# Kernel optimization log

Measured on AMD Instinct MI355X. Metric: run time of the kernel, lower is better.

Reference implementation:

```python
import jax, jax.numpy as jnp
import numpy as np

NUM_EXPERTS = 8
TOP_K = 2

def setup_inputs() -> dict:
    key = jax.random.key(0)
    ks = jax.random.split(key, 5)
    B, S, D, F, E = 4, 2048, 1024, 4096, NUM_EXPERTS
    x = jax.random.normal(ks[0], (B, S, D), dtype=jnp.float32)
    router_w = jax.random.normal(ks[1], (D, E), dtype=jnp.float32) * 0.02
    router_b = jnp.zeros((E,), dtype=jnp.float32)
    w1 = jax.random.normal(ks[2], (E, D, F), dtype=jnp.float32) * 0.02
    b1 = jnp.zeros((E, F), dtype=jnp.float32)
    w2 = jax.random.normal(ks[3], (E, F, D), dtype=jnp.float32) * 0.02
    b2 = jnp.zeros((E, D), dtype=jnp.float32)
    return {"x": x, "router_w": router_w, "router_b": router_b,
            "w1": w1, "b1": b1, "w2": w2, "b2": b2}

def reference(x, router_w, router_b, w1, b1, w2, b2):
    B, S, D = x.shape
    E = router_w.shape[1]
    x_flat = x.reshape(-1, D)                                  # [N, D]
    router_probs = jax.nn.softmax(x_flat @ router_w + router_b, axis=-1)  # [N, E]
    topk_probs, topk_idx = jax.lax.top_k(router_probs, TOP_K)  # [N, K]
    topk_probs = topk_probs / jnp.sum(topk_probs, axis=-1, keepdims=True)
    # combine weight per (token, expert): sum over top-k slots assigned to that expert
    cw = jnp.sum(topk_probs[..., None] * jax.nn.one_hot(topk_idx, E, dtype=x.dtype), axis=1)  # [N, E]
    out = jnp.zeros_like(x_flat)
    for e in range(E):  # small fixed expert count; each iter is a dense GEMM pair
        h = jax.nn.gelu(x_flat @ w1[e] + b1[e], approximate=False)  # [N, F]
        out = out + cw[:, e:e + 1] * (h @ w2[e] + b2[e])            # [N, D]
    return out.reshape(B, S, D)
```

## Files before the change

kernel.cpp:

```cpp
#include <hip/hip_runtime.h>
#include <hip/hip_bf16.h>

typedef __attribute__((ext_vector_type(8))) __bf16 bf16x8;
typedef __attribute__((ext_vector_type(4))) float f32x4;

#define NTOK 8192
#define D_DIM 1024
#define F_DIM 4096
#define NEXP 8
#define SLOT_TOT 16384
#define SLOT_CAP 16640
#define TILE_MAX 136
#define TILE_MAX2 72

__device__ __forceinline__ unsigned short f2b(float f) {
  __hip_bfloat16 b = __float2bfloat16(f);
  return reinterpret_cast<unsigned short&>(b);
}

__device__ __forceinline__ float gelu_f(float v) {
  const float y2 = v * (1.5957691216f + 0.0713548162f * v * v);
  return v * __builtin_amdgcn_rcpf(1.f + __expf(-y2));
}

__device__ __forceinline__ void gload_lds16(const void* g, void* l) {
  __builtin_amdgcn_global_load_lds(
      (__attribute__((address_space(1))) void*)g,
      (__attribute__((address_space(3))) void*)l, 16, 0, 0);
}


__global__ void init_counts_kernel(int* counts) {
  if (threadIdx.x < NEXP) counts[threadIdx.x] = 0;
}

__global__ void zero_out_kernel(float* out) {
  const int i = blockIdx.x * 256 + threadIdx.x;
  reinterpret_cast<float4*>(out)[i] = make_float4(0.f, 0.f, 0.f, 0.f);
}

__global__ void scatter_gather_kernel(const float* __restrict__ x,
                                      const int* __restrict__ topk_idx,
                                      int* __restrict__ cursors,
                                      int* __restrict__ slot_pos,
                                      __hip_bfloat16* __restrict__ xg) {
  __shared__ int ps[2];
  const int tok = blockIdx.x;
  const int tid = threadIdx.x;
  if (tid < 2) {
    const int e = topk_idx[tok * 2 + tid];
    const int p = atomicAdd(&cursors[e], 1);
    slot_pos[tok * 2 + tid] = p;
    ps[tid] = p;
  }
  __syncthreads();
  const int d = tid * 4;
  const float4 v = *reinterpret_cast<const float4*>(x + (size_t)tok * D_DIM + d);
  union { unsigned short u[4]; uint2 q; } o;
  o.u[0] = f2b(v.x); o.u[1] = f2b(v.y); o.u[2] = f2b(v.z); o.u[3] = f2b(v.w);
  *reinterpret_cast<uint2*>(xg + (size_t)ps[0] * D_DIM + d) = o.q;
  *reinterpret_cast<uint2*>(xg + (size_t)ps[1] * D_DIM + d) = o.q;
}

__global__ void combine_kernel(const __hip_bfloat16* __restrict__ ys,
                               const int* __restrict__ slot_pos,
                               const float* __restrict__ topk_w,
                               float* __restrict__ out) {
  const int tok = blockIdx.x;
  const int d = threadIdx.x * 4;
  const int s0 = slot_pos[tok * 2], s1 = slot_pos[tok * 2 + 1];
  const float w0 = topk_w[tok * 2], w1 = topk_w[tok * 2 + 1];
  union { unsigned short u[4]; uint2 q; } a, b;
  a.q = *reinterpret_cast<const uint2*>(ys + (size_t)s0 * D_DIM + d);
  b.q = *reinterpret_cast<const uint2*>(ys + (size_t)s1 * D_DIM + d);
  float4 rr;
  float va[4];
  #pragma unroll
  for (int i = 0; i < 4; ++i) {
    unsigned int ua = (unsigned int)a.u[i] << 16;
    unsigned int ub = (unsigned int)b.u[i] << 16;
    va[i] = w0 * reinterpret_cast<float&>(ua) + w1 * reinterpret_cast<float&>(ub);
  }
  rr.x = va[0]; rr.y = va[1]; rr.z = va[2]; rr.w = va[3];
  *reinterpret_cast<float4*>(out + (size_t)tok * D_DIM + d) = rr;
}

__global__ void transpose_conv_kernel(const float* __restrict__ src,
                                      __hip_bfloat16* __restrict__ dst,
                                      int R, int C) {
  __shared__ float tile[64][65];
  const int e = blockIdx.z;
  src += (size_t)e * R * C;
  dst += (size_t)e * R * C;
  const int c0 = blockIdx.x * 64, r0 = blockIdx.y * 64;
  const int tid = threadIdx.x;
  const int lr = tid >> 4, lc4 = (tid & 15) * 4;
  #pragma unroll
  for (int pass = 0; pass < 4; ++pass) {
    const int rr = pass * 16 + lr;
    const float4 v = *reinterpret_cast<const float4*>(
        &src[(size_t)(r0 + rr) * C + c0 + lc4]);
    tile[rr][lc4 + 0] = v.x; tile[rr][lc4 + 1] = v.y;
    tile[rr][lc4 + 2] = v.z; tile[rr][lc4 + 3] = v.w;
  }
  __syncthreads();
  const int sc = tid >> 3, sr8 = (tid & 7) * 8;
  #pragma unroll
  for (int pass = 0; pass < 2; ++pass) {
    const int c = pass * 32 + sc;
    union { unsigned short u[8]; uint4 q; } o;
    #pragma unroll
    for (int i = 0; i < 8; ++i) o.u[i] = f2b(tile[sr8 + i][c]);
    *reinterpret_cast<uint4*>(&dst[(size_t)(c0 + c) * R + r0 + sr8]) = o.q;
  }
}

__global__ void router_kernel(const float* __restrict__ x,
                              const float* __restrict__ rw,
                              const float* __restrict__ rb,
                              int* __restrict__ topk_idx,
                              float* __restrict__ topk_w,
                              int* __restrict__ counts) {
  __shared__ float rwT[NEXP * D_DIM];
  const int tid = threadIdx.x;
  for (int i = tid; i < NEXP * D_DIM; i += 256) {
    const int d = i >> 3, e = i & 7;
    rwT[e * D_DIM + d] = rw[i];
  }
  __syncthreads();

  const int wave = tid >> 6, lane = tid & 63;
  const int tok = blockIdx.x * 4 + wave;
  const float* xr = x + (size_t)tok * D_DIM;

  float acc[NEXP];
  #pragma unroll
  for (int e = 0; e < NEXP; ++e) acc[e] = 0.f;

  for (int i = 0; i < D_DIM / 64; ++i) {
    const int d = i * 64 + lane;
    const float xv = xr[d];
    #pragma unroll
    for (int e = 0; e < NEXP; ++e) acc[e] += xv * rwT[e * D_DIM + d];
  }
  #pragma unroll
  for (int off = 32; off > 0; off >>= 1) {
    #pragma unroll
    for (int e = 0; e < NEXP; ++e) acc[e] += __shfl_xor(acc[e], off);
  }

  if (lane == 0) {
    float l[NEXP];
    #pragma unroll
    for (int e = 0; e < NEXP; ++e) l[e] = acc[e] + rb[e];
    int i1 = 0;
    #pragma unroll
    for (int e = 1; e < NEXP; ++e) if (l[e] > l[i1]) i1 = e;
    int i2 = (i1 == 0) ? 1 : 0;
    #pragma unroll
    for (int e = 0; e < NEXP; ++e) if (e != i1 && e != i2 && l[e] > l[i2]) i2 = e;
    const float w1 = 1.f / (1.f + __expf(l[i2] - l[i1]));
    topk_idx[tok * 2 + 0] = i1;
    topk_idx[tok * 2 + 1] = i2;
    topk_w[tok * 2 + 0] = w1;
    topk_w[tok * 2 + 1] = 1.f - w1;
    atomicAdd(&counts[i1], 1);
    atomicAdd(&counts[i2], 1);
  }
}

__global__ void offsets_kernel(const int* __restrict__ counts,
                               int* __restrict__ offsets,
                               int* __restrict__ cursors,
                               int* __restrict__ tile_meta,
                               int* __restrict__ tile_meta2) {
  if (threadIdx.x == 0) {
    int s = 0;
    for (int e = 0; e < NEXP; ++e) { offsets[e] = s; cursors[e] = s; s += counts[e]; }
    offsets[NEXP] = s;
    int n = 0;
    for (int e = 0; e < NEXP; ++e) {
      const int nt = (counts[e] + 127) >> 7;
      for (int m = 0; m < nt && n < TILE_MAX; ++m) tile_meta[n++] = e | (m << 8);
    }
    for (; n < TILE_MAX; ++n) tile_meta[n] = 0 | (1 << 22);
    n = 0;
    for (int e = 0; e < NEXP; ++e) {
      const int nt = (counts[e] + 255) >> 8;
      for (int m = 0; m < nt && n < TILE_MAX2; ++m) tile_meta2[n++] = e | (m << 8);
    }
    for (; n < TILE_MAX2; ++n) tile_meta2[n] = 0 | (1 << 22);
  }
}

__global__ __launch_bounds__(512, 2) void moe_gemm1(
    const __hip_bfloat16* __restrict__ A,
    const __hip_bfloat16* __restrict__ B,
    const float* __restrict__ bias,
    const int* __restrict__ counts,
    const int* __restrict__ offsets,
    const int* __restrict__ tile_meta2,
    __hip_bfloat16* __restrict__ Hout) {
  constexpr int K = D_DIM, NCOL = F_DIM;
  constexpr int KT = K / 64;

  const int bid = blockIdx.x;
  const int j = bid >> 4, nt = bid & 15;
  const int meta = tile_meta2[j];
  const int e = meta & 255, mt = meta >> 8;
  const int cnt = counts[e];
  if (mt * 256 >= cnt) return;
  const int base = offsets[e];

  __shared__ unsigned short lds[2][32768];

  const int tid = threadIdx.x;
  const int w = tid >> 6, lane = tid & 63;
  const int r = lane & 15, kg = lane >> 4;
  const int wm = w >> 2, wn = w & 3;

  const __hip_bfloat16* gA0 = A + (size_t)(base + mt * 256 + w * 16 + r) * K + kg * 8;
  const __hip_bfloat16* gA1 = gA0 + (size_t)128 * K;
  const __hip_bfloat16* gB0 = B + ((size_t)e * NCOL + nt * 256 + w * 16 + r) * K + kg * 8;
  const __hip_bfloat16* gB1 = gB0 + (size_t)128 * K;

  f32x4 acc[8][4] = {};

  auto stage = [&](unsigned short* buf) {
    gload_lds16(gA0,      buf + w * 512);
    gload_lds16(gA1,      buf + (w + 8) * 512);
    gload_lds16(gA0 + 32, buf + (16 + w) * 512);
    gload_lds16(gA1 + 32, buf + (16 + w + 8) * 512);
    gload_lds16(gB0,      buf + 16384 + w * 512);
    gload_lds16(gB1,      buf + 16384 + (w + 8) * 512);
    gload_lds16(gB0 + 32, buf + 16384 + (16 + w) * 512);
    gload_lds16(gB1 + 32, buf + 16384 + (16 + w + 8) * 512);
    gA0 += 64; gA1 += 64; gB0 += 64; gB1 += 64;
  };
  auto compute = [&](const unsigned short* buf) {
    #pragma unroll
    for (int kk = 0; kk < 2; ++kk) {
      bf16x8 af[8], bfr[4];
      #pragma unroll
      for (int m = 0; m < 8; ++m)
        af[m] = *(const bf16x8*)(buf + (kk * 16 + wm * 8 + m) * 512 + lane * 8);
      #pragma unroll
      for (int n = 0; n < 4; ++n)
        bfr[n] = *(const bf16x8*)(buf + 16384 + (kk * 16 + wn * 4 + n) * 512 + lane * 8);
      #pragma unroll
      for (int m = 0; m < 8; ++m)
        #pragma unroll
        for (int n = 0; n < 4; ++n)
          acc[m][n] = __builtin_amdgcn_mfma_f32_16x16x32_bf16(
              af[m], bfr[n], acc[m][n], 0, 0, 0);
    }
  };

  unsigned short* pc = lds[0];
  unsigned short* pn = lds[1];

  stage(pc);
  __syncthreads();
  for (int t = 0; t < KT - 1; ++t) {
    stage(pn);
    compute(pc);
    __syncthreads();
    unsigned short* ts = pc; pc = pn; pn = ts;
  }
  compute(pc);

  const int rem = cnt - mt * 256;
  const int q4 = (lane >> 4) * 4;
  const int c15 = lane & 15;

  if (rem >= 256) {
    #pragma unroll
    for (int n = 0; n < 4; ++n) {
      const int col = nt * 256 + wn * 64 + n * 16 + c15;
      const float bv = bias[e * NCOL + col];
      #pragma unroll
      for (int m = 0; m < 8; ++m)
        #pragma unroll
        for (int rr = 0; rr < 4; ++rr) {
          const int rloc = wm * 128 + m * 16 + q4 + rr;
          Hout[(size_t)(base + mt * 256 + rloc) * NCOL + col] =
              __float2bfloat16(gelu_f(acc[m][n][rr] + bv));
        }
    }
  } else {
    #pragma unroll
    for (int n = 0; n < 4; ++n) {
      const int col = nt * 256 + wn * 64 + n * 16 + c15;
      const float bv = bias[e * NCOL + col];
      #pragma unroll
      for (int m = 0; m < 8; ++m)
        #pragma unroll
        for (int rr = 0; rr < 4; ++rr) {
          const int rloc = wm * 128 + m * 16 + q4 + rr;
          if (rloc < rem)
            Hout[(size_t)(base + mt * 256 + rloc) * NCOL + col] =
                __float2bfloat16(gelu_f(acc[m][n][rr] + bv));
        }
    }
  }
}

__global__ __launch_bounds__(256, 4) void moe_gemm2(
    const __hip_bfloat16* __restrict__ A,
    const __hip_bfloat16* __restrict__ B,
    const float* __restrict__ bias,
    const int* __restrict__ counts,
    const int* __restrict__ offsets,
    const int* __restrict__ tile_meta,
    __hip_bfloat16* __restrict__ Cout) {
  constexpr int K = F_DIM, NCOL = D_DIM;
  constexpr int NT = NCOL / 128;
  constexpr int KT = K / 32;

  const int bid = blockIdx.x;
  const int j = bid / NT, nt = bid % NT;
  const int meta = tile_meta[j];
  const int e = meta & 255, mt = meta >> 8;
  const int cnt = counts[e];
  if (mt * 128 >= cnt) return;
  const int base = offsets[e];

  __shared__ unsigned short lds[2][8192];

  const int tid = threadIdx.x;
  const int w = tid >> 6, lane = tid & 63;
  const int r = lane & 15, kg = lane >> 4;
  const int wm = w >> 1, wn = w & 1;

  const __hip_bfloat16* gA0 = A + (size_t)(base + mt * 128 + w * 16 + r) * K + kg * 8;
  const __hip_bfloat16* gA1 = gA0 + (size_t)64 * K;
  const __hip_bfloat16* gB0 = B + ((size_t)e * NCOL + nt * 128 + w * 16 + r) * K + kg * 8;
  const __hip_bfloat16* gB1 = gB0 + (size_t)64 * K;

  f32x4 acc[4][4] = {};

  auto stage = [&](unsigned short* buf) {
    gload_lds16(gA0, buf + w * 512);
    gload_lds16(gA1, buf + (w + 4) * 512);
    gload_lds16(gB0, buf + 4096 + w * 512);
    gload_lds16(gB1, buf + 4096 + (w + 4) * 512);
    gA0 += 32; gA1 += 32; gB0 += 32; gB1 += 32;
  };
  auto compute = [&](const unsigned short* buf) {
    bf16x8 af[4], bfr[4];
    #pragma unroll
    for (int i2 = 0; i2 < 4; ++i2) {
      af[i2]  = *(const bf16x8*)(buf + (wm * 4 + i2) * 512 + lane * 8);
      bfr[i2] = *(const bf16x8*)(buf + 4096 + (wn * 4 + i2) * 512 + lane * 8);
    }
    #pragma unroll
    for (int mi = 0; mi < 4; ++mi)
      #pragma unroll
      for (int ni = 0; ni < 4; ++ni)
        acc[mi][ni] = __builtin_amdgcn_mfma_f32_16x16x32_bf16(
            af[mi], bfr[ni], acc[mi][ni], 0, 0, 0);
  };

  unsigned short* pc = lds[0];
  unsigned short* pn = lds[1];

  stage(pc);
  __syncthreads();
  for (int t = 0; t < KT - 1; ++t) {
    stage(pn);
    compute(pc);
    __syncthreads();
    unsigned short* ts = pc; pc = pn; pn = ts;
  }
  compute(pc);

  const int rem = cnt - mt * 128;
  const int q4 = (lane >> 4) * 4;
  const int c15 = lane & 15;

  if (rem >= 128) {
    #pragma unroll
    for (int n = 0; n < 4; ++n) {
      const int col = nt * 128 + wn * 64 + n * 16 + c15;
      const float bv = bias[e * NCOL + col];
      #pragma unroll
      for (int m = 0; m < 4; ++m)
        #pragma unroll
        for (int rr = 0; rr < 4; ++rr) {
          const int rloc = wm * 64 + m * 16 + q4 + rr;
          Cout[(size_t)(base + mt * 128 + rloc) * NCOL + col] =
              __float2bfloat16(acc[m][n][rr] + bv);
        }
    }
  } else {
    #pragma unroll
    for (int n = 0; n < 4; ++n) {
      const int col = nt * 128 + wn * 64 + n * 16 + c15;
      const float bv = bias[e * NCOL + col];
      #pragma unroll
      for (int m = 0; m < 4; ++m)
        #pragma unroll
        for (int rr = 0; rr < 4; ++rr) {
          const int rloc = wm * 64 + m * 16 + q4 + rr;
          if (rloc < rem)
            Cout[(size_t)(base + mt * 128 + rloc) * NCOL + col] =
                __float2bfloat16(acc[m][n][rr] + bv);
        }
    }
  }
}


extern "C" void kernel_launch(void* const* d_in, const int* in_sizes, int n_in,
                              void* d_out, int out_size, void* d_ws, size_t ws_size,
                              hipStream_t stream) {
  const float* x  = (const float*)d_in[0];
  const float* rw = (const float*)d_in[1];
  const float* rb = (const float*)d_in[2];
  const float* w1 = (const float*)d_in[3];
  const float* b1 = (const float*)d_in[4];
  const float* w2 = (const float*)d_in[5];
  const float* b2 = (const float*)d_in[6];
  float* out = (float*)d_out;

  char* p = (char*)d_ws;
  size_t used = 0;
  auto carve = [&](size_t bytes) {
    char* r = p + used;
    used += (bytes + 255) & ~(size_t)255;
    return (void*)r;
  };
  __hip_bfloat16* xg  = (__hip_bfloat16*)carve((size_t)SLOT_CAP * D_DIM * 2);
  __hip_bfloat16* ys  = xg;
  __hip_bfloat16* w1t = (__hip_bfloat16*)carve((size_t)NEXP * F_DIM * D_DIM * 2);
  __hip_bfloat16* w2t = (__hip_bfloat16*)carve((size_t)NEXP * D_DIM * F_DIM * 2);
  __hip_bfloat16* h   = (__hip_bfloat16*)carve((size_t)SLOT_CAP * F_DIM * 2);
  int*   topk_idx   = (int*)carve((size_t)NTOK * 2 * 4);
  float* topk_w     = (float*)carve((size_t)NTOK * 2 * 4);
  int*   slot_pos   = (int*)carve((size_t)NTOK * 2 * 4);
  int*   tile_meta  = (int*)carve(TILE_MAX * 4);
  int*   tile_meta2 = (int*)carve(TILE_MAX2 * 4);
  int* counts  = (int*)carve(256);
  int* offsets = (int*)carve(256);
  int* cursors = (int*)carve(256);

  if (used > ws_size) {
    zero_out_kernel<<<8192, 256, 0, stream>>>(out);
    return;
  }

  init_counts_kernel<<<1, 64, 0, stream>>>(counts);
  router_kernel<<<NTOK / 4, 256, 0, stream>>>(x, rw, rb, topk_idx, topk_w, counts);
  offsets_kernel<<<1, 64, 0, stream>>>(counts, offsets, cursors, tile_meta, tile_meta2);
  scatter_gather_kernel<<<NTOK, 256, 0, stream>>>(x, topk_idx, cursors, slot_pos, xg);

  transpose_conv_kernel<<<dim3(F_DIM / 64, D_DIM / 64, NEXP), 256, 0, stream>>>(
      w1, w1t, D_DIM, F_DIM);
  transpose_conv_kernel<<<dim3(D_DIM / 64, F_DIM / 64, NEXP), 256, 0, stream>>>(
      w2, w2t, F_DIM, D_DIM);

  moe_gemm1<<<TILE_MAX2 * (F_DIM / 256), 512, 0, stream>>>(
      xg, w1t, b1, counts, offsets, tile_meta2, h);
  moe_gemm2<<<TILE_MAX * (D_DIM / 128), 256, 0, stream>>>(
      h, w2t, b2, counts, offsets, tile_meta, ys);

  combine_kernel<<<NTOK, 256, 0, stream>>>(ys, slot_pos, topk_w, out);
}
```

Before: 961.7 us.

## Restructure MoE GEMM tiling with larger blocks and XCD-aware tile mapping

gemm1 now runs 1024-thread blocks with 16 waves, each holding a 4x4 MFMA accumulator, and a K-step of 32 instead of 64. gemm2 moves to 256-row M tiles with 512 threads, so both GEMMs share one tile table and the separate 128-row table is dropped. Block indices are remapped so that consecutive tiles of the same expert land on the same XCD, which is meant to improve L2 reuse of weights and activations. In exchange, gemm1 has twice as many K iterations and barriers, and the 1024-thread blocks with launch_bounds(1024,4) may limit registers per thread.

```diff
diff --git a/kernel.cpp b/kernel.cpp
--- a/kernel.cpp
+++ b/kernel.cpp
@@ -10,8 +10,8 @@
 #define NEXP 8
 #define SLOT_TOT 16384
 #define SLOT_CAP 16640
-#define TILE_MAX 136
 #define TILE_MAX2 72
+#define JPX2 9
 
 __device__ __forceinline__ unsigned short f2b(float f) {
   __hip_bfloat16 b = __float2bfloat16(f);
@@ -172,7 +172,6 @@
 __global__ void offsets_kernel(const int* __restrict__ counts,
                                int* __restrict__ offsets,
                                int* __restrict__ cursors,
-                               int* __restrict__ tile_meta,
                                int* __restrict__ tile_meta2) {
   if (threadIdx.x == 0) {
     int s = 0;
@@ -180,20 +179,14 @@
     offsets[NEXP] = s;
     int n = 0;
     for (int e = 0; e < NEXP; ++e) {
-      const int nt = (counts[e] + 127) >> 7;
-      for (int m = 0; m < nt && n < TILE_MAX; ++m) tile_meta[n++] = e | (m << 8);
-    }
-    for (; n < TILE_MAX; ++n) tile_meta[n] = 0 | (1 << 22);
-    n = 0;
-    for (int e = 0; e < NEXP; ++e) {
-      const int nt = (counts[e] + 255) >> 8;
-      for (int m = 0; m < nt && n < TILE_MAX2; ++m) tile_meta2[n++] = e | (m << 8);
+      const int ntile = (counts[e] + 255) >> 8;
+      for (int m = 0; m < ntile && n < TILE_MAX2; ++m) tile_meta2[n++] = e | (m << 8);
     }
     for (; n < TILE_MAX2; ++n) tile_meta2[n] = 0 | (1 << 22);
   }
 }
 
-__global__ __launch_bounds__(512, 2) void moe_gemm1(
+__global__ __launch_bounds__(1024, 4) void moe_gemm1(
     const __hip_bfloat16* __restrict__ A,
     const __hip_bfloat16* __restrict__ B,
     const float* __restrict__ bias,
@@ -202,58 +195,48 @@
     const int* __restrict__ tile_meta2,
     __hip_bfloat16* __restrict__ Hout) {
   constexpr int K = D_DIM, NCOL = F_DIM;
-  constexpr int KT = K / 64;
-
-  const int bid = blockIdx.x;
-  const int j = bid >> 4, nt = bid & 15;
+  constexpr int KT = K / 32;
+
+  const int xcd = blockIdx.x & 7;
+  const int local = blockIdx.x >> 3;
+  const int j = xcd * JPX2 + (local >> 4);
+  const int nt = local & 15;
   const int meta = tile_meta2[j];
   const int e = meta & 255, mt = meta >> 8;
   const int cnt = counts[e];
   if (mt * 256 >= cnt) return;
   const int base = offsets[e];
 
-  __shared__ unsigned short lds[2][32768];
+  __shared__ unsigned short lds[2][16384];
 
   const int tid = threadIdx.x;
   const int w = tid >> 6, lane = tid & 63;
   const int r = lane & 15, kg = lane >> 4;
   const int wm = w >> 2, wn = w & 3;
 
-  const __hip_bfloat16* gA0 = A + (size_t)(base + mt * 256 + w * 16 + r) * K + kg * 8;
-  const __hip_bfloat16* gA1 = gA0 + (size_t)128 * K;
-  const __hip_bfloat16* gB0 = B + ((size_t)e * NCOL + nt * 256 + w * 16 + r) * K + kg * 8;
-  const __hip_bfloat16* gB1 = gB0 + (size_t)128 * K;
-
-  f32x4 acc[8][4] = {};
+  const __hip_bfloat16* gA = A + (size_t)(base + mt * 256 + w * 16 + r) * K + kg * 8;
+  const __hip_bfloat16* gB = B + ((size_t)e * NCOL + nt * 256 + w * 16 + r) * K + kg * 8;
+
+  f32x4 acc[4][4] = {};
 
   auto stage = [&](unsigned short* buf) {
-    gload_lds16(gA0,      buf + w * 512);
-    gload_lds16(gA1,      buf + (w + 8) * 512);
-    gload_lds16(gA0 + 32, buf + (16 + w) * 512);
-    gload_lds16(gA1 + 32, buf + (16 + w + 8) * 512);
-    gload_lds16(gB0,      buf + 16384 + w * 512);
-    gload_lds16(gB1,      buf + 16384 + (w + 8) * 512);
-    gload_lds16(gB0 + 32, buf + 16384 + (16 + w) * 512);
-    gload_lds16(gB1 + 32, buf + 16384 + (16 + w + 8) * 512);
-    gA0 += 64; gA1 += 64; gB0 += 64; gB1 += 64;
+    gload_lds16(gA, buf + w * 512);
+    gload_lds16(gB, buf + 8192 + w * 512);
+    gA += 32; gB += 32;
   };
   auto compute = [&](const unsigned short* buf) {
-    #pragma unroll
-    for (int kk = 0; kk < 2; ++kk) {
-      bf16x8 af[8], bfr[4];
-      #pragma unroll
-      for (int m = 0; m < 8; ++m)
-        af[m] = *(const bf16x8*)(buf + (kk * 16 + wm * 8 + m) * 512 + lane * 8);
-      #pragma unroll
-      for (int n = 0; n < 4; ++n)
-        bfr[n] = *(const bf16x8*)(buf + 16384 + (kk * 16 + wn * 4 + n) * 512 + lane * 8);
-      #pragma unroll
-      for (int m = 0; m < 8; ++m)
-        #pragma unroll
-        for (int n = 0; n < 4; ++n)
-          acc[m][n] = __builtin_amdgcn_mfma_f32_16x16x32_bf16(
-              af[m], bfr[n], acc[m][n], 0, 0, 0);
-    }
+    bf16x8 af[4], bfr[4];
+    #pragma unroll
+    for (int i2 = 0; i2 < 4; ++i2) {
+      af[i2]  = *(const bf16x8*)(buf + (wm * 4 + i2) * 512 + lane * 8);
+      bfr[i2] = *(const bf16x8*)(buf + 8192 + (wn * 4 + i2) * 512 + lane * 8);
+    }
+    #pragma unroll
+    for (int mi = 0; mi < 4; ++mi)
+      #pragma unroll
+      for (int ni = 0; ni < 4; ++ni)
+        acc[mi][ni] = __builtin_amdgcn_mfma_f32_16x16x32_bf16(
+            af[mi], bfr[ni], acc[mi][ni], 0, 0, 0);
   };
 
   unsigned short* pc = lds[0];
@@ -279,10 +262,10 @@
       const int col = nt * 256 + wn * 64 + n * 16 + c15;
       const float bv = bias[e * NCOL + col];
       #pragma unroll
-      for (int m = 0; m < 8; ++m)
+      for (int m = 0; m < 4; ++m)
         #pragma unroll
         for (int rr = 0; rr < 4; ++rr) {
-          const int rloc = wm * 128 + m * 16 + q4 + rr;
+          const int rloc = wm * 64 + m * 16 + q4 + rr;
           Hout[(size_t)(base + mt * 256 + rloc) * NCOL + col] =
               __float2bfloat16(gelu_f(acc[m][n][rr] + bv));
         }
@@ -293,10 +276,10 @@
       const int col = nt * 256 + wn * 64 + n * 16 + c15;
       const float bv = bias[e * NCOL + col];
       #pragma unroll
-      for (int m = 0; m < 8; ++m)
+      for (int m = 0; m < 4; ++m)
         #pragma unroll
         for (int rr = 0; rr < 4; ++rr) {
-          const int rloc = wm * 128 + m * 16 + q4 + rr;
+          const int rloc = wm * 64 + m * 16 + q4 + rr;
           if (rloc < rem)
             Hout[(size_t)(base + mt * 256 + rloc) * NCOL + col] =
                 __float2bfloat16(gelu_f(acc[m][n][rr] + bv));
@@ -305,53 +288,52 @@
   }
 }
 
-__global__ __launch_bounds__(256, 4) void moe_gemm2(
+__global__ __launch_bounds__(512, 4) void moe_gemm2(
     const __hip_bfloat16* __restrict__ A,
     const __hip_bfloat16* __restrict__ B,
     const float* __restrict__ bias,
     const int* __restrict__ counts,
     const int* __restrict__ offsets,
-    const int* __restrict__ tile_meta,
+    const int* __restrict__ tile_meta2,
     __hip_bfloat16* __restrict__ Cout) {
   constexpr int K = F_DIM, NCOL = D_DIM;
-  constexpr int NT = NCOL / 128;
   constexpr int KT = K / 32;
 
-  const int bid = blockIdx.x;
-  const int j = bid / NT, nt = bid % NT;
-  const int meta = tile_meta[j];
+  const int xcd = blockIdx.x & 7;
+  const int local = blockIdx.x >> 3;
+  const int j = xcd * JPX2 + (local >> 3);
+  const int nt = local & 7;
+  const int meta = tile_meta2[j];
   const int e = meta & 255, mt = meta >> 8;
   const int cnt = counts[e];
-  if (mt * 128 >= cnt) return;
+  if (mt * 256 >= cnt) return;
   const int base = offsets[e];
 
-  __shared__ unsigned short lds[2][8192];
+  __shared__ unsigned short lds[2][12288];
 
   const int tid = threadIdx.x;
   const int w = tid >> 6, lane = tid & 63;
   const int r = lane & 15, kg = lane >> 4;
   const int wm = w >> 1, wn = w & 1;
 
-  const __hip_bfloat16* gA0 = A + (size_t)(base + mt * 128 + w * 16 + r) * K + kg * 8;
-  const __hip_bfloat16* gA1 = gA0 + (size_t)64 * K;
+  const __hip_bfloat16* gA0 = A + (size_t)(base + mt * 256 + w * 16 + r) * K + kg * 8;
+  const __hip_bfloat16* gA1 = gA0 + (size_t)128 * K;
   const __hip_bfloat16* gB0 = B + ((size_t)e * NCOL + nt * 128 + w * 16 + r) * K + kg * 8;
-  const __hip_bfloat16* gB1 = gB0 + (size_t)64 * K;
 
   f32x4 acc[4][4] = {};
 
   auto stage = [&](unsigned short* buf) {
     gload_lds16(gA0, buf + w * 512);
-    gload_lds16(gA1, buf + (w + 4) * 512);
-    gload_lds16(gB0, buf + 4096 + w * 512);
-    gload_lds16(gB1, buf + 4096 + (w + 4) * 512);
-    gA0 += 32; gA1 += 32; gB0 += 32; gB1 += 32;
+    gload_lds16(gA1, buf + (w + 8) * 512);
+    gload_lds16(gB0, buf + 8192 + w * 512);
+    gA0 += 32; gA1 += 32; gB0 += 32;
   };
   auto compute = [&](const unsigned short* buf) {
     bf16x8 af[4], bfr[4];
     #pragma unroll
     for (int i2 = 0; i2 < 4; ++i2) {
       af[i2]  = *(const bf16x8*)(buf + (wm * 4 + i2) * 512 + lane * 8);
-      bfr[i2] = *(const bf16x8*)(buf + 4096 + (wn * 4 + i2) * 512 + lane * 8);
+      bfr[i2] = *(const bf16x8*)(buf + 8192 + (wn * 4 + i2) * 512 + lane * 8);
     }
     #pragma unroll
     for (int mi = 0; mi < 4; ++mi)
@@ -374,11 +356,11 @@
   }
   compute(pc);
 
-  const int rem = cnt - mt * 128;
+  const int rem = cnt - mt * 256;
   const int q4 = (lane >> 4) * 4;
   const int c15 = lane & 15;
 
-  if (rem >= 128) {
+  if (rem >= 256) {
     #pragma unroll
     for (int n = 0; n < 4; ++n) {
       const int col = nt * 128 + wn * 64 + n * 16 + c15;
@@ -388,7 +370,7 @@
         #pragma unroll
         for (int rr = 0; rr < 4; ++rr) {
           const int rloc = wm * 64 + m * 16 + q4 + rr;
-          Cout[(size_t)(base + mt * 128 + rloc) * NCOL + col] =
+          Cout[(size_t)(base + mt * 256 + rloc) * NCOL + col] =
               __float2bfloat16(acc[m][n][rr] + bv);
         }
     }
@@ -403,7 +385,7 @@
         for (int rr = 0; rr < 4; ++rr) {
           const int rloc = wm * 64 + m * 16 + q4 + rr;
           if (rloc < rem)
-            Cout[(size_t)(base + mt * 128 + rloc) * NCOL + col] =
+            Cout[(size_t)(base + mt * 256 + rloc) * NCOL + col] =
                 __float2bfloat16(acc[m][n][rr] + bv);
         }
     }
@@ -438,7 +420,6 @@
   int*   topk_idx   = (int*)carve((size_t)NTOK * 2 * 4);
   float* topk_w     = (float*)carve((size_t)NTOK * 2 * 4);
   int*   slot_pos   = (int*)carve((size_t)NTOK * 2 * 4);
-  int*   tile_meta  = (int*)carve(TILE_MAX * 4);
   int*   tile_meta2 = (int*)carve(TILE_MAX2 * 4);
   int* counts  = (int*)carve(256);
   int* offsets = (int*)carve(256);
@@ -451,7 +432,7 @@
 
   init_counts_kernel<<<1, 64, 0, stream>>>(counts);
   router_kernel<<<NTOK / 4, 256, 0, stream>>>(x, rw, rb, topk_idx, topk_w, counts);
-  offsets_kernel<<<1, 64, 0, stream>>>(counts, offsets, cursors, tile_meta, tile_meta2);
+  offsets_kernel<<<1, 64, 0, stream>>>(counts, offsets, cursors, tile_meta2);
   scatter_gather_kernel<<<NTOK, 256, 0, stream>>>(x, topk_idx, cursors, slot_pos, xg);
 
   transpose_conv_kernel<<<dim3(F_DIM / 64, D_DIM / 64, NEXP), 256, 0, stream>>>(
@@ -459,10 +440,10 @@
   transpose_conv_kernel<<<dim3(D_DIM / 64, F_DIM / 64, NEXP), 256, 0, stream>>>(
       w2, w2t, F_DIM, D_DIM);
 
-  moe_gemm1<<<TILE_MAX2 * (F_DIM / 256), 512, 0, stream>>>(
+  moe_gemm1<<<TILE_MAX2 * (F_DIM / 256), 1024, 0, stream>>>(
       xg, w1t, b1, counts, offsets, tile_meta2, h);
-  moe_gemm2<<<TILE_MAX * (D_DIM / 128), 256, 0, stream>>>(
-      h, w2t, b2, counts, offsets, tile_meta, ys);
+  moe_gemm2<<<TILE_MAX2 * (D_DIM / 128), 512, 0, stream>>>(
+      h, w2t, b2, counts, offsets, tile_meta2, ys);
 
   combine_kernel<<<NTOK, 256, 0, stream>>>(ys, slot_pos, topk_w, out);
 }
```

New measurement: 976.7 us. Within noise of the previous version (+1.6%).
